# Optimization experiments

Hardware: AMD Instinct MI355X
Metric: run time of the kernel (lower is better)

Reference implementation:

```python
import jax, jax.numpy as jnp
import numpy as np

B, N, DIM = 4, 2048, 512
H, DH = 8, 64  # n_heads, dim_head; inner = H*DH = 512
SCALE = DH ** -0.5


def setup_inputs() -> dict:
    key = jax.random.key(0)
    k1, k2, k3 = jax.random.split(key, 3)
    inner = H * DH
    X = jax.random.normal(k1, (B, N, DIM), dtype=jnp.float32)
    W_qkv = jax.random.normal(k2, (DIM, 3 * inner), dtype=jnp.float32) * (DIM ** -0.5)
    W_out = jax.random.normal(k3, (inner, DIM), dtype=jnp.float32) * (inner ** -0.5)
    b_out = jnp.zeros((DIM,), dtype=jnp.float32)
    return {"X": X, "W_qkv": W_qkv, "W_out": W_out, "b_out": b_out}


def reference(X, W_qkv, W_out, b_out):
    # X: (b, n, dim)
    qkv = X @ W_qkv                      # (b, n, 3*h*d)
    q, k, v = jnp.split(qkv, 3, axis=-1)
    def to_heads(t):
        b, n, _ = t.shape
        return t.reshape(b, n, H, DH).transpose(0, 2, 1, 3)  # (b, h, n, d)
    q, k, v = to_heads(q), to_heads(k), to_heads(v)
    # NOTE: original computes scores[n, m] = k_n . q_m and softmaxes over m (query axis)
    scores = jnp.einsum('bhnd,bhmd->bhnm', k, q) * SCALE     # (b, h, n_k, m_q)
    att = jax.nn.softmax(scores, axis=-1)
    # out token axis is the KEY index n: out[n, d] = sum_e att[n, e] * v[e, d]
    out = jnp.einsum('bhne,bhed->bhnd', att, v)              # (b, h, n, d)
    out = out.transpose(0, 2, 1, 3).reshape(X.shape[0], X.shape[1], H * DH)  # (b, n, h*d)
    return out @ W_out + b_out
```

## Files before the change

### kernel.cpp

```cpp
#include <hip/hip_runtime.h>
#include <hip/hip_bf16.h>

typedef __bf16 bf16_t;
typedef bf16_t bf16x8 __attribute__((ext_vector_type(8)));
typedef bf16_t bf16x4v __attribute__((ext_vector_type(4)));
typedef float f32x4 __attribute__((ext_vector_type(4)));
typedef float f32x16 __attribute__((ext_vector_type(16)));
typedef int i32x4 __attribute__((ext_vector_type(4)));

#define B_SZ 4
#define N_TOK 2048
#define DIM 512
#define H_N 8
#define DH 64
#define INNER 512
#define M_ROWS 8192
#define NQKV 1536
#define K_FOLD 0.18033688011112042f

#define GLD_LDS16(gp, lp)                                          \
  __builtin_amdgcn_global_load_lds(                                \
      (const __attribute__((address_space(1))) void*)(gp),         \
      (__attribute__((address_space(3))) void*)(lp), 16, 0, 0)

__device__ __forceinline__ float fexp2(float x) {
#if __has_builtin(__builtin_amdgcn_exp2f)
  return __builtin_amdgcn_exp2f(x);
#else
  float r;
  asm volatile("v_exp_f32 %0, %1\n\ts_nop 1" : "=v"(r) : "v"(x));
  return r;
#endif
}

__device__ __forceinline__ int cvtpk_bf16(float lo, float hi) {
  int r;
  asm("v_cvt_pk_bf16_f32 %0, %1, %2" : "=v"(r) : "v"(lo), "v"(hi));
  return r;
}

__device__ __forceinline__ void permswap32(int& a, int& b) {
  asm volatile("v_permlane32_swap_b32 %0, %1" : "+v"(a), "+v"(b));
}

__global__ __launch_bounds__(256) void prep_kernel(
    const float* __restrict__ X, bf16_t* __restrict__ Xb,
    const float* __restrict__ Wqkv, bf16_t* __restrict__ WqkvT,
    const float* __restrict__ Wout, bf16_t* __restrict__ WoutT) {
  __shared__ float t[64][65];
  const int bid = blockIdx.x, tid = threadIdx.x;

  if (bid < 2048) {
    int i = bid * 256 + tid;
    float4 f0 = reinterpret_cast<const float4*>(X)[2 * i];
    float4 f1 = reinterpret_cast<const float4*>(X)[2 * i + 1];
    bf16x8 o;
    o[0] = (bf16_t)f0.x; o[1] = (bf16_t)f0.y; o[2] = (bf16_t)f0.z; o[3] = (bf16_t)f0.w;
    o[4] = (bf16_t)f1.x; o[5] = (bf16_t)f1.y; o[6] = (bf16_t)f1.z; o[7] = (bf16_t)f1.w;
    reinterpret_cast<bf16x8*>(Xb)[i] = o;
    return;
  }

  int tb = bid - 2048;
  const float* src;
  bf16_t* dst;
  int C, r0, c0;
  if (tb < 192) {
    src = Wqkv; dst = WqkvT; C = NQKV;
    r0 = (tb / 24) * 64; c0 = (tb % 24) * 64;
  } else {
    tb -= 192;
    src = Wout; dst = WoutT; C = DIM;
    r0 = (tb >> 3) * 64; c0 = (tb & 7) * 64;
  }

  #pragma unroll
  for (int p = 0; p < 4; ++p) {
    int idx = p * 256 + tid;
    int tr = idx >> 4, tc = (idx & 15) * 4;
    float4 v = *reinterpret_cast<const float4*>(&src[(size_t)(r0 + tr) * C + c0 + tc]);
    t[tr][tc] = v.x; t[tr][tc + 1] = v.y; t[tr][tc + 2] = v.z; t[tr][tc + 3] = v.w;
  }
  __syncthreads();
  #pragma unroll
  for (int p = 0; p < 2; ++p) {
    int idx = p * 256 + tid;
    int d = idx >> 3, j8 = idx & 7;
    bf16x8 o;
    #pragma unroll
    for (int q = 0; q < 8; ++q) o[q] = (bf16_t)t[j8 * 8 + q][d];
    *reinterpret_cast<bf16x8*>(&dst[(size_t)(c0 + d) * 512 + r0 + j8 * 8]) = o;
  }
}

__global__ __launch_bounds__(256) void gemm_qkv_kernel(
    const bf16_t* __restrict__ A, const bf16_t* __restrict__ Bt, int K,
    bf16_t* __restrict__ qb, bf16_t* __restrict__ kb, bf16_t* __restrict__ vtb) {
  __shared__ bf16_t As[128 * 64];
  __shared__ bf16_t Bs[128 * 64];

  const int tid = threadIdx.x;
  const int lane = tid & 63;
  const int wave = tid >> 6;
  const int g = lane >> 4, c = lane & 15;
  const int wm = (wave >> 1) * 64, wn = (wave & 1) * 64;
  const int m0 = blockIdx.x * 128, n0 = blockIdx.y * 128;

  f32x4 acc[4][4] = {};

  for (int k0 = 0; k0 < K; k0 += 64) {
    __syncthreads();
    #pragma unroll
    for (int i = 0; i < 4; ++i) {
      int blk = i * 256 + tid;
      int row = blk >> 3;
      int cb = (blk & 7) ^ (row & 7);
      int base = (i * 256 + wave * 64) * 8;
      GLD_LDS16(A + (size_t)(m0 + row) * K + k0 + cb * 8, &As[base]);
      GLD_LDS16(Bt + (size_t)(n0 + row) * K + k0 + cb * 8, &Bs[base]);
    }
    __syncthreads();
    __builtin_amdgcn_s_setprio(1);
    #pragma unroll
    for (int ks = 0; ks < 2; ++ks) {
      bf16x8 af[4], bfr[4];
      #pragma unroll
      for (int i = 0; i < 4; ++i) {
        af[i] = *reinterpret_cast<const bf16x8*>(
            &As[(wm + i * 16 + c) * 64 + (((ks * 4 + g) ^ (c & 7)) * 8)]);
        bfr[i] = *reinterpret_cast<const bf16x8*>(
            &Bs[(wn + i * 16 + c) * 64 + (((ks * 4 + g) ^ (c & 7)) * 8)]);
      }
      #pragma unroll
      for (int mi = 0; mi < 4; ++mi)
        #pragma unroll
        for (int ni = 0; ni < 4; ++ni)
          acc[mi][ni] = __builtin_amdgcn_mfma_f32_16x16x32_bf16(
              af[mi], bfr[ni], acc[mi][ni], 0, 0, 0);
    }
    __builtin_amdgcn_s_setprio(0);
  }

  #pragma unroll
  for (int mi = 0; mi < 4; ++mi) {
    #pragma unroll
    for (int ni = 0; ni < 4; ++ni) {
      int colg = n0 + wn + ni * 16 + c;
      int s = colg >> 9;
      int hh = (colg >> 6) & 7, dd = colg & 63;
      int rowg0 = m0 + wm + mi * 16 + g * 4;
      int bb = rowg0 >> 11, nn = rowg0 & 2047;
      if (s == 2) {
        bf16x4v pk;
        pk.x = (bf16_t)acc[mi][ni][0];
        pk.y = (bf16_t)acc[mi][ni][1];
        pk.z = (bf16_t)acc[mi][ni][2];
        pk.w = (bf16_t)acc[mi][ni][3];
        *reinterpret_cast<bf16x4v*>(
            &vtb[(((size_t)(bb * H_N + hh)) * DH + dd) * N_TOK + nn]) = pk;
      } else {
        float sc = (s == 1) ? K_FOLD : 1.0f;
        bf16_t* dst = (s == 0) ? qb : kb;
        #pragma unroll
        for (int r = 0; r < 4; ++r)
          dst[(((size_t)(bb * H_N + hh)) * N_TOK + nn + r) * DH + dd] =
              (bf16_t)(acc[mi][ni][r] * sc);
      }
    }
  }
}

__global__ __launch_bounds__(256) void gemm_out_kernel(
    const bf16_t* __restrict__ A, const bf16_t* __restrict__ Bt,
    float* __restrict__ outF, const float* __restrict__ bias) {
  __shared__ bf16_t As[64 * 64];
  __shared__ bf16_t Bs[128 * 64];

  const int tid = threadIdx.x;
  const int lane = tid & 63;
  const int wave = tid >> 6;
  const int g = lane >> 4, c = lane & 15;
  const int wm = (wave >> 1) * 32, wn = (wave & 1) * 64;
  const int m0 = blockIdx.x * 64, n0 = blockIdx.y * 128;

  f32x4 acc[2][4] = {};

  for (int k0 = 0; k0 < DIM; k0 += 64) {
    __syncthreads();
    #pragma unroll
    for (int i = 0; i < 2; ++i) {
      int blk = i * 256 + tid;
      int row = blk >> 3;
      int cb = (blk & 7) ^ (row & 7);
      int base = (i * 256 + wave * 64) * 8;
      GLD_LDS16(A + (size_t)(m0 + row) * DIM + k0 + cb * 8, &As[base]);
    }
    #pragma unroll
    for (int i = 0; i < 4; ++i) {
      int blk = i * 256 + tid;
      int row = blk >> 3;
      int cb = (blk & 7) ^ (row & 7);
      int base = (i * 256 + wave * 64) * 8;
      GLD_LDS16(Bt + (size_t)(n0 + row) * DIM + k0 + cb * 8, &Bs[base]);
    }
    __syncthreads();
    __builtin_amdgcn_s_setprio(1);
    #pragma unroll
    for (int ks = 0; ks < 2; ++ks) {
      bf16x8 af[2], bfr[4];
      #pragma unroll
      for (int i = 0; i < 2; ++i)
        af[i] = *reinterpret_cast<const bf16x8*>(
            &As[(wm + i * 16 + c) * 64 + (((ks * 4 + g) ^ (c & 7)) * 8)]);
      #pragma unroll
      for (int i = 0; i < 4; ++i)
        bfr[i] = *reinterpret_cast<const bf16x8*>(
            &Bs[(wn + i * 16 + c) * 64 + (((ks * 4 + g) ^ (c & 7)) * 8)]);
      #pragma unroll
      for (int mi = 0; mi < 2; ++mi)
        #pragma unroll
        for (int ni = 0; ni < 4; ++ni)
          acc[mi][ni] = __builtin_amdgcn_mfma_f32_16x16x32_bf16(
              af[mi], bfr[ni], acc[mi][ni], 0, 0, 0);
    }
    __builtin_amdgcn_s_setprio(0);
  }

  #pragma unroll
  for (int mi = 0; mi < 2; ++mi) {
    #pragma unroll
    for (int ni = 0; ni < 4; ++ni) {
      int colg = n0 + wn + ni * 16 + c;
      #pragma unroll
      for (int r = 0; r < 4; ++r) {
        int rowg = m0 + wm + mi * 16 + g * 4 + r;
        outF[(size_t)rowg * DIM + colg] = acc[mi][ni][r] + bias[colg];
      }
    }
  }
}

__global__ __launch_bounds__(512, 4) void attn_kernel(
    const bf16_t* __restrict__ Qproj, const bf16_t* __restrict__ Kproj,
    const bf16_t* __restrict__ Vt, bf16_t* __restrict__ att_out) {
  const int glin = blockIdx.x;
  const int xcd = glin & 7;
  const int jj = glin >> 3;
  const int hb = xcd * 4 + (jj >> 4);
  const int rb = jj & 15;
  const int h = hb & 7, b = hb >> 3;

  const size_t hbo = (size_t)(b * H_N + h);
  const bf16_t* Aq = Kproj + hbo * N_TOK * DH;
  const bf16_t* Ak = Qproj + hbo * N_TOK * DH;
  const bf16_t* Av = Vt + hbo * (size_t)(DH * N_TOK);

  const int tid = threadIdx.x, lane = tid & 63, wave = tid >> 6;
  const int nl = lane & 31;
  const int hf = lane >> 5;
  const int grp = wave >> 2;
  const int gw = wave & 3;
  const int r0 = rb * 128, wr0 = gw * 32;
  const int kv0 = grp * 1024;

  __shared__ __align__(16) char smem[65536];
  bf16_t* sKg = (bf16_t*)(smem + grp * 32768);
  bf16_t* sVg = (bf16_t*)(smem + grp * 32768 + 16384);

  bf16x8 qreg[4];
  #pragma unroll
  for (int ks = 0; ks < 4; ++ks)
    qreg[ks] = *reinterpret_cast<const bf16x8*>(
        &Aq[(size_t)(r0 + wr0 + nl) * DH + ks * 16 + hf * 8]);

  f32x16 accO0 = {}, accO1 = {};
  float Lp[4] = {};

  const int gtid = tid & 255;
  auto stage = [&](int buf, int j0) {
    #pragma unroll
    for (int i = 0; i < 2; ++i) {
      int idx = i * 256 + gtid;
      int row = idx >> 3;
      int cb = (idx & 7) ^ (row & 7);
      int base = buf * 4096 + (i * 256 + gw * 64) * 8;
      GLD_LDS16(Ak + (size_t)(j0 + row) * DH + cb * 8, sKg + base);
      GLD_LDS16(Av + (size_t)row * N_TOK + j0 + cb * 8, sVg + base);
    }
  };

  stage(0, kv0);
  __syncthreads();

  constexpr int NT = 16;
  for (int t = 0; t < NT; ++t) {
    if (t + 1 < NT) stage((t + 1) & 1, kv0 + (t + 1) * 64);
    const bf16_t* bK = sKg + (t & 1) * 4096;
    const bf16_t* bV = sVg + (t & 1) * 4096;

    f32x16 aT[2] = {};
    __builtin_amdgcn_s_setprio(1);
    #pragma unroll
    for (int ks = 0; ks < 4; ++ks) {
      #pragma unroll
      for (int mi = 0; mi < 2; ++mi) {
        int rowt = mi * 32 + nl;
        bf16x8 ak = *reinterpret_cast<const bf16x8*>(
            &bK[rowt * 64 + (((ks * 2 + hf) ^ (rowt & 7)) * 8)]);
        aT[mi] = __builtin_amdgcn_mfma_f32_32x32x16_bf16(
            ak, qreg[ks], aT[mi], 0, 0, 0);
      }
    }
    __builtin_amdgcn_s_setprio(0);

    #pragma unroll
    for (int r = 0; r < 16; ++r) {
      float p0 = fexp2(aT[0][r]); aT[0][r] = p0;
      float p1 = fexp2(aT[1][r]); aT[1][r] = p1;
      Lp[r & 3] += p0 + p1;
    }

    i32x4 pk[4];
    #pragma unroll
    for (int ks = 0; ks < 4; ++ks) {
      const int mi = ks >> 1, base = (ks & 1) * 8;
      int a0 = cvtpk_bf16(aT[mi][base + 0], aT[mi][base + 1]);
      int b0 = cvtpk_bf16(aT[mi][base + 4], aT[mi][base + 5]);
      int a1 = cvtpk_bf16(aT[mi][base + 2], aT[mi][base + 3]);
      int b1 = cvtpk_bf16(aT[mi][base + 6], aT[mi][base + 7]);
      permswap32(a0, b0);
      permswap32(a1, b1);
      pk[ks].x = a0; pk[ks].y = a1; pk[ks].z = b0; pk[ks].w = b1;
    }

    __builtin_amdgcn_s_setprio(1);
    #pragma unroll
    for (int ks = 0; ks < 4; ++ks) {
      bf16x8 pfrag = __builtin_bit_cast(bf16x8, pk[ks]);
      int rv0 = nl, rv1 = 32 + nl;
      bf16x8 av0 = *reinterpret_cast<const bf16x8*>(
          &bV[rv0 * 64 + (((ks * 2 + hf) ^ (rv0 & 7)) * 8)]);
      bf16x8 av1 = *reinterpret_cast<const bf16x8*>(
          &bV[rv1 * 64 + (((ks * 2 + hf) ^ (rv1 & 7)) * 8)]);
      accO0 = __builtin_amdgcn_mfma_f32_32x32x16_bf16(av0, pfrag, accO0, 0, 0, 0);
      accO1 = __builtin_amdgcn_mfma_f32_32x32x16_bf16(av1, pfrag, accO1, 0, 0, 0);
    }
    __builtin_amdgcn_s_setprio(0);

    __syncthreads();
  }

  float Lsum = (Lp[0] + Lp[1]) + (Lp[2] + Lp[3]);
  float* mb = (float*)smem;
  const int moff = (gw * 64 + lane) * 37;
  if (grp == 1) {
    #pragma unroll
    for (int r = 0; r < 16; ++r) {
      mb[moff + r] = accO0[r];
      mb[moff + 16 + r] = accO1[r];
    }
    mb[moff + 32] = Lsum;
  }
  __syncthreads();
  if (grp == 0) {
    #pragma unroll
    for (int r = 0; r < 16; ++r) {
      accO0[r] += mb[moff + r];
      accO1[r] += mb[moff + 16 + r];
    }
    float l = Lsum + mb[moff + 32];
    l += __shfl_xor(l, 32);
    float invL = 1.0f / l;
    const int nrow = r0 + wr0 + nl;
    #pragma unroll
    for (int q = 0; q < 4; ++q) {
      int d0a = 8 * q + 4 * hf;
      bf16x4v o;
      o.x = (bf16_t)(accO0[4 * q + 0] * invL);
      o.y = (bf16_t)(accO0[4 * q + 1] * invL);
      o.z = (bf16_t)(accO0[4 * q + 2] * invL);
      o.w = (bf16_t)(accO0[4 * q + 3] * invL);
      *reinterpret_cast<bf16x4v*>(
          &att_out[((size_t)(b * N_TOK) + nrow) * INNER + h * DH + d0a]) = o;
      bf16x4v o2;
      o2.x = (bf16_t)(accO1[4 * q + 0] * invL);
      o2.y = (bf16_t)(accO1[4 * q + 1] * invL);
      o2.z = (bf16_t)(accO1[4 * q + 2] * invL);
      o2.w = (bf16_t)(accO1[4 * q + 3] * invL);
      *reinterpret_cast<bf16x4v*>(
          &att_out[((size_t)(b * N_TOK) + nrow) * INNER + h * DH + 32 + d0a]) = o2;
    }
  }
}


extern "C" void kernel_launch(void* const* d_in, const int* in_sizes, int n_in,
                              void* d_out, int out_size, void* d_ws, size_t ws_size,
                              hipStream_t stream) {
  const float* X    = (const float*)d_in[0];
  const float* Wqkv = (const float*)d_in[1];
  const float* Wout = (const float*)d_in[2];
  const float* bout = (const float*)d_in[3];
  float* out = (float*)d_out;

  char* ws = (char*)d_ws;
  bf16_t* Xb    = (bf16_t*)(ws);
  bf16_t* WqkvT = (bf16_t*)(ws + 8388608);
  bf16_t* WoutT = (bf16_t*)(ws + 9961472);
  bf16_t* Qb    = (bf16_t*)(ws + 10485760);
  bf16_t* Kb    = (bf16_t*)(ws + 18874368);
  bf16_t* Vtb   = (bf16_t*)(ws + 27262976);
  bf16_t* AttO  = (bf16_t*)(ws + 35651584);

  prep_kernel<<<dim3(2304), 256, 0, stream>>>(X, Xb, Wqkv, WqkvT, Wout, WoutT);

  dim3 g1(M_ROWS / 128, NQKV / 128);
  gemm_qkv_kernel<<<g1, 256, 0, stream>>>(Xb, WqkvT, DIM, Qb, Kb, Vtb);

  attn_kernel<<<dim3(512), 512, 0, stream>>>(Qb, Kb, Vtb, AttO);

  dim3 g3(M_ROWS / 64, DIM / 128);
  gemm_out_kernel<<<g3, 256, 0, stream>>>(AttO, WoutT, out, bout);
}
```

Before: 79.51 us.

## Fuse X fp32-to-bf16 conversion into QKV GEMM and stage V transpose via LDS

Result: slower. 91.14 us (+14.6%).

```diff
diff --git a/kernel.cpp b/kernel.cpp
--- a/kernel.cpp
+++ b/kernel.cpp
@@ -44,24 +44,11 @@
 }
 
 __global__ __launch_bounds__(256) void prep_kernel(
-    const float* __restrict__ X, bf16_t* __restrict__ Xb,
     const float* __restrict__ Wqkv, bf16_t* __restrict__ WqkvT,
     const float* __restrict__ Wout, bf16_t* __restrict__ WoutT) {
   __shared__ float t[64][65];
-  const int bid = blockIdx.x, tid = threadIdx.x;
-
-  if (bid < 2048) {
-    int i = bid * 256 + tid;
-    float4 f0 = reinterpret_cast<const float4*>(X)[2 * i];
-    float4 f1 = reinterpret_cast<const float4*>(X)[2 * i + 1];
-    bf16x8 o;
-    o[0] = (bf16_t)f0.x; o[1] = (bf16_t)f0.y; o[2] = (bf16_t)f0.z; o[3] = (bf16_t)f0.w;
-    o[4] = (bf16_t)f1.x; o[5] = (bf16_t)f1.y; o[6] = (bf16_t)f1.z; o[7] = (bf16_t)f1.w;
-    reinterpret_cast<bf16x8*>(Xb)[i] = o;
-    return;
-  }
-
-  int tb = bid - 2048;
+  int tb = blockIdx.x;
+  const int tid = threadIdx.x;
   const float* src;
   bf16_t* dst;
   int C, r0, c0;
@@ -94,10 +81,11 @@
 }
 
 __global__ __launch_bounds__(256) void gemm_qkv_kernel(
-    const bf16_t* __restrict__ A, const bf16_t* __restrict__ Bt, int K,
+    const float* __restrict__ Af, const bf16_t* __restrict__ Bt,
     bf16_t* __restrict__ qb, bf16_t* __restrict__ kb, bf16_t* __restrict__ vtb) {
-  __shared__ bf16_t As[128 * 64];
-  __shared__ bf16_t Bs[128 * 64];
+  __shared__ __align__(16) char smem[36864];
+  bf16_t* As = (bf16_t*)smem;
+  bf16_t* Bs = (bf16_t*)(smem + 16384);
 
   const int tid = threadIdx.x;
   const int lane = tid & 63;
@@ -108,7 +96,7 @@
 
   f32x4 acc[4][4] = {};
 
-  for (int k0 = 0; k0 < K; k0 += 64) {
+  for (int k0 = 0; k0 < DIM; k0 += 64) {
     __syncthreads();
     #pragma unroll
     for (int i = 0; i < 4; ++i) {
@@ -116,8 +104,21 @@
       int row = blk >> 3;
       int cb = (blk & 7) ^ (row & 7);
       int base = (i * 256 + wave * 64) * 8;
-      GLD_LDS16(A + (size_t)(m0 + row) * K + k0 + cb * 8, &As[base]);
-      GLD_LDS16(Bt + (size_t)(n0 + row) * K + k0 + cb * 8, &Bs[base]);
+      GLD_LDS16(Bt + (size_t)(n0 + row) * DIM + k0 + cb * 8, &Bs[base]);
+    }
+    #pragma unroll
+    for (int i = 0; i < 4; ++i) {
+      int blk = i * 256 + tid;
+      int row = blk >> 3, lb = blk & 7;
+      const float* sp = &Af[(size_t)(m0 + row) * DIM + k0 + lb * 8];
+      float4 f0 = *reinterpret_cast<const float4*>(sp);
+      float4 f1 = *reinterpret_cast<const float4*>(sp + 4);
+      i32x4 w;
+      w.x = cvtpk_bf16(f0.x, f0.y);
+      w.y = cvtpk_bf16(f0.z, f0.w);
+      w.z = cvtpk_bf16(f1.x, f1.y);
+      w.w = cvtpk_bf16(f1.z, f1.w);
+      *reinterpret_cast<i32x4*>(&As[row * 64 + ((lb ^ (row & 7)) * 8)]) = w;
     }
     __syncthreads();
     __builtin_amdgcn_s_setprio(1);
@@ -136,36 +137,56 @@
         #pragma unroll
         for (int ni = 0; ni < 4; ++ni)
           acc[mi][ni] = __builtin_amdgcn_mfma_f32_16x16x32_bf16(
-              af[mi], bfr[ni], acc[mi][ni], 0, 0, 0);
+              bfr[ni], af[mi], acc[mi][ni], 0, 0, 0);
     }
     __builtin_amdgcn_s_setprio(0);
   }
 
-  #pragma unroll
-  for (int mi = 0; mi < 4; ++mi) {
-    #pragma unroll
-    for (int ni = 0; ni < 4; ++ni) {
-      int colg = n0 + wn + ni * 16 + c;
-      int s = colg >> 9;
-      int hh = (colg >> 6) & 7, dd = colg & 63;
-      int rowg0 = m0 + wm + mi * 16 + g * 4;
-      int bb = rowg0 >> 11, nn = rowg0 & 2047;
-      if (s == 2) {
-        bf16x4v pk;
-        pk.x = (bf16_t)acc[mi][ni][0];
-        pk.y = (bf16_t)acc[mi][ni][1];
-        pk.z = (bf16_t)acc[mi][ni][2];
-        pk.w = (bf16_t)acc[mi][ni][3];
-        *reinterpret_cast<bf16x4v*>(
-            &vtb[(((size_t)(bb * H_N + hh)) * DH + dd) * N_TOK + nn]) = pk;
-      } else {
+  if (n0 < 1024) {
+    #pragma unroll
+    for (int mi = 0; mi < 4; ++mi) {
+      #pragma unroll
+      for (int ni = 0; ni < 4; ++ni) {
+        int rowg = m0 + wm + mi * 16 + c;
+        int colg0 = n0 + wn + ni * 16 + g * 4;
+        int s = colg0 >> 9;
+        int hh = (colg0 >> 6) & 7, dd = colg0 & 63;
+        int bb = rowg >> 11, nn = rowg & 2047;
         float sc = (s == 1) ? K_FOLD : 1.0f;
         bf16_t* dst = (s == 0) ? qb : kb;
+        bf16x4v pk;
+        pk.x = (bf16_t)(acc[mi][ni][0] * sc);
+        pk.y = (bf16_t)(acc[mi][ni][1] * sc);
+        pk.z = (bf16_t)(acc[mi][ni][2] * sc);
+        pk.w = (bf16_t)(acc[mi][ni][3] * sc);
+        *reinterpret_cast<bf16x4v*>(
+            &dst[(((size_t)(bb * H_N + hh)) * N_TOK + nn) * DH + dd]) = pk;
+      }
+    }
+  } else {
+    __syncthreads();
+    bf16_t* T = (bf16_t*)smem;
+    #pragma unroll
+    for (int mi = 0; mi < 4; ++mi)
+      #pragma unroll
+      for (int ni = 0; ni < 4; ++ni) {
+        int cl = wn + ni * 16 + g * 4;
+        int tl = wm + mi * 16 + c;
         #pragma unroll
         for (int r = 0; r < 4; ++r)
-          dst[(((size_t)(bb * H_N + hh)) * N_TOK + nn + r) * DH + dd] =
-              (bf16_t)(acc[mi][ni][r] * sc);
+          T[(cl + r) * 132 + tl] = (bf16_t)acc[mi][ni][r];
       }
+    __syncthreads();
+    const int bb = m0 >> 11, nn0 = m0 & 2047;
+    #pragma unroll
+    for (int p = 0; p < 8; ++p) {
+      int q8 = p * 256 + tid;
+      int dl = q8 >> 4, t8 = (q8 & 15) * 8;
+      bf16x8 o = *reinterpret_cast<const bf16x8*>(&T[dl * 132 + t8]);
+      int ddb = n0 - 1024 + dl;
+      int hh = ddb >> 6, ddh = ddb & 63;
+      *reinterpret_cast<bf16x8*>(
+          &vtb[((size_t)(bb * H_N + hh) * DH + ddh) * N_TOK + nn0 + t8]) = o;
     }
   }
 }
@@ -404,7 +425,6 @@
   float* out = (float*)d_out;
 
   char* ws = (char*)d_ws;
-  bf16_t* Xb    = (bf16_t*)(ws);
   bf16_t* WqkvT = (bf16_t*)(ws + 8388608);
   bf16_t* WoutT = (bf16_t*)(ws + 9961472);
   bf16_t* Qb    = (bf16_t*)(ws + 10485760);
@@ -412,10 +432,10 @@
   bf16_t* Vtb   = (bf16_t*)(ws + 27262976);
   bf16_t* AttO  = (bf16_t*)(ws + 35651584);
 
-  prep_kernel<<<dim3(2304), 256, 0, stream>>>(X, Xb, Wqkv, WqkvT, Wout, WoutT);
+  prep_kernel<<<dim3(256), 256, 0, stream>>>(Wqkv, WqkvT, Wout, WoutT);
 
   dim3 g1(M_ROWS / 128, NQKV / 128);
-  gemm_qkv_kernel<<<g1, 256, 0, stream>>>(Xb, WqkvT, DIM, Qb, Kb, Vtb);
+  gemm_qkv_kernel<<<g1, 256, 0, stream>>>(X, WqkvT, Qb, Kb, Vtb);
 
   attn_kernel<<<dim3(512), 512, 0, stream>>>(Qb, Kb, Vtb, AttO);
 
```

## Halve attention KV tile to 32 and shrink LDS to raise occupancy

Applied to the files above, without the earlier changes.

Result: slower. 272.5 us (+242.7%).

```diff
diff --git a/kernel.cpp b/kernel.cpp
--- a/kernel.cpp
+++ b/kernel.cpp
@@ -240,7 +240,7 @@
   }
 }
 
-__global__ __launch_bounds__(512, 4) void attn_kernel(
+__global__ __launch_bounds__(512, 8) void attn_kernel(
     const bf16_t* __restrict__ Qproj, const bf16_t* __restrict__ Kproj,
     const bf16_t* __restrict__ Vt, bf16_t* __restrict__ att_out) {
   const int glin = blockIdx.x;
@@ -263,9 +263,9 @@
   const int r0 = rb * 128, wr0 = gw * 32;
   const int kv0 = grp * 1024;
 
-  __shared__ __align__(16) char smem[65536];
-  bf16_t* sKg = (bf16_t*)(smem + grp * 32768);
-  bf16_t* sVg = (bf16_t*)(smem + grp * 32768 + 16384);
+  __shared__ __align__(16) char smem[38912];
+  bf16_t* sKg = (bf16_t*)(smem + grp * 16384);
+  bf16_t* sVg = (bf16_t*)(smem + grp * 16384 + 8192);
 
   bf16x8 qreg[4];
   #pragma unroll
@@ -277,71 +277,56 @@
   float Lp[4] = {};
 
   const int gtid = tid & 255;
+  const int rowK = gtid >> 3, cbK = (gtid & 7) ^ ((gtid >> 3) & 7);
+  const int rowV = gtid >> 2, pV = (gtid & 3) ^ ((gtid >> 2) & 3);
   auto stage = [&](int buf, int j0) {
-    #pragma unroll
-    for (int i = 0; i < 2; ++i) {
-      int idx = i * 256 + gtid;
-      int row = idx >> 3;
-      int cb = (idx & 7) ^ (row & 7);
-      int base = buf * 4096 + (i * 256 + gw * 64) * 8;
-      GLD_LDS16(Ak + (size_t)(j0 + row) * DH + cb * 8, sKg + base);
-      GLD_LDS16(Av + (size_t)row * N_TOK + j0 + cb * 8, sVg + base);
-    }
+    int base = buf * 2048 + gw * 512;
+    GLD_LDS16(Ak + (size_t)(j0 + rowK) * DH + cbK * 8, sKg + base);
+    GLD_LDS16(Av + (size_t)rowV * N_TOK + j0 + pV * 8, sVg + base);
   };
 
   stage(0, kv0);
   __syncthreads();
 
-  constexpr int NT = 16;
+  constexpr int NT = 32;
   for (int t = 0; t < NT; ++t) {
-    if (t + 1 < NT) stage((t + 1) & 1, kv0 + (t + 1) * 64);
-    const bf16_t* bK = sKg + (t & 1) * 4096;
-    const bf16_t* bV = sVg + (t & 1) * 4096;
-
-    f32x16 aT[2] = {};
+    if (t + 1 < NT) stage((t + 1) & 1, kv0 + (t + 1) * 32);
+    const bf16_t* bK = sKg + (t & 1) * 2048;
+    const bf16_t* bV = sVg + (t & 1) * 2048;
+
+    f32x16 aT = {};
     __builtin_amdgcn_s_setprio(1);
     #pragma unroll
     for (int ks = 0; ks < 4; ++ks) {
-      #pragma unroll
-      for (int mi = 0; mi < 2; ++mi) {
-        int rowt = mi * 32 + nl;
-        bf16x8 ak = *reinterpret_cast<const bf16x8*>(
-            &bK[rowt * 64 + (((ks * 2 + hf) ^ (rowt & 7)) * 8)]);
-        aT[mi] = __builtin_amdgcn_mfma_f32_32x32x16_bf16(
-            ak, qreg[ks], aT[mi], 0, 0, 0);
-      }
+      bf16x8 ak = *reinterpret_cast<const bf16x8*>(
+          &bK[nl * 64 + (((ks * 2 + hf) ^ (nl & 7)) * 8)]);
+      aT = __builtin_amdgcn_mfma_f32_32x32x16_bf16(ak, qreg[ks], aT, 0, 0, 0);
     }
     __builtin_amdgcn_s_setprio(0);
 
     #pragma unroll
     for (int r = 0; r < 16; ++r) {
-      float p0 = fexp2(aT[0][r]); aT[0][r] = p0;
-      float p1 = fexp2(aT[1][r]); aT[1][r] = p1;
-      Lp[r & 3] += p0 + p1;
-    }
-
-    i32x4 pk[4];
-    #pragma unroll
-    for (int ks = 0; ks < 4; ++ks) {
-      const int mi = ks >> 1, base = (ks & 1) * 8;
-      int a0 = cvtpk_bf16(aT[mi][base + 0], aT[mi][base + 1]);
-      int b0 = cvtpk_bf16(aT[mi][base + 4], aT[mi][base + 5]);
-      int a1 = cvtpk_bf16(aT[mi][base + 2], aT[mi][base + 3]);
-      int b1 = cvtpk_bf16(aT[mi][base + 6], aT[mi][base + 7]);
+      float p = fexp2(aT[r]);
+      aT[r] = p;
+      Lp[r & 3] += p;
+    }
+
+    __builtin_amdgcn_s_setprio(1);
+    #pragma unroll
+    for (int ks2 = 0; ks2 < 2; ++ks2) {
+      const int base = ks2 * 8;
+      int a0 = cvtpk_bf16(aT[base + 0], aT[base + 1]);
+      int b0 = cvtpk_bf16(aT[base + 4], aT[base + 5]);
+      int a1 = cvtpk_bf16(aT[base + 2], aT[base + 3]);
+      int b1 = cvtpk_bf16(aT[base + 6], aT[base + 7]);
       permswap32(a0, b0);
       permswap32(a1, b1);
-      pk[ks].x = a0; pk[ks].y = a1; pk[ks].z = b0; pk[ks].w = b1;
-    }
-
-    __builtin_amdgcn_s_setprio(1);
-    #pragma unroll
-    for (int ks = 0; ks < 4; ++ks) {
-      bf16x8 pfrag = __builtin_bit_cast(bf16x8, pk[ks]);
-      int rv0 = nl, rv1 = 32 + nl;
+      i32x4 w; w.x = a0; w.y = a1; w.z = b0; w.w = b1;
+      bf16x8 pfrag = __builtin_bit_cast(bf16x8, w);
       bf16x8 av0 = *reinterpret_cast<const bf16x8*>(
-          &bV[rv0 * 64 + (((ks * 2 + hf) ^ (rv0 & 7)) * 8)]);
+          &bV[nl * 32 + (((ks2 * 2 + hf) ^ (nl & 3)) * 8)]);
       bf16x8 av1 = *reinterpret_cast<const bf16x8*>(
-          &bV[rv1 * 64 + (((ks * 2 + hf) ^ (rv1 & 7)) * 8)]);
+          &bV[(32 + nl) * 32 + (((ks2 * 2 + hf) ^ (nl & 3)) * 8)]);
       accO0 = __builtin_amdgcn_mfma_f32_32x32x16_bf16(av0, pfrag, accO0, 0, 0, 0);
       accO1 = __builtin_amdgcn_mfma_f32_32x32x16_bf16(av1, pfrag, accO1, 0, 0, 0);
     }
```
